# Kernel tuning notes

Measured on AMD Instinct MI355X. Metric: run time of the kernel, lower is better.

The kernel has to match this reference:

```python
import jax, jax.numpy as jnp
import numpy as np

BN_EPS = 1e-5


def setup_inputs() -> dict:
    key = jax.random.key(0)
    ks = jax.random.split(key, 6)
    n, c, h, w = 16, 256, 80, 80
    mip = max(8, c // 32)  # reduction=32 -> mip=8
    x = jax.random.normal(ks[0], (n, c, h, w), dtype=jnp.float32)
    # 1x1 conv weights (bias=False), stored as [out_ch, in_ch]
    w_fc = jax.random.normal(ks[1], (mip, c), dtype=jnp.float32) * (1.0 / np.sqrt(c))
    w_h = jax.random.normal(ks[2], (c, mip), dtype=jnp.float32) * (1.0 / np.sqrt(mip))
    w_w = jax.random.normal(ks[3], (c, mip), dtype=jnp.float32) * (1.0 / np.sqrt(mip))
    # BatchNorm2d(mip) inference params
    bn_gamma = jnp.ones((mip,), dtype=jnp.float32)
    bn_beta = jnp.zeros((mip,), dtype=jnp.float32)
    bn_mean = jax.random.normal(ks[4], (mip,), dtype=jnp.float32) * 0.1
    bn_var = jax.random.uniform(ks[5], (mip,), dtype=jnp.float32, minval=0.5, maxval=1.5)
    return {"x": x, "w_fc": w_fc, "bn_gamma": bn_gamma, "bn_beta": bn_beta,
            "bn_mean": bn_mean, "bn_var": bn_var, "w_h": w_h, "w_w": w_w}


def reference(x, w_fc, bn_gamma, bn_beta, bn_mean, bn_var, w_h, w_w):
    n, c, h, w = x.shape
    # Adaptive pools: pool_h -> mean over W (n,c,h); pool_w -> mean over H (n,c,w)
    x_h = jnp.mean(x, axis=3)  # (n, c, h)
    x_w = jnp.mean(x, axis=2)  # (n, c, w)
    # concat along the length axis (equiv. to torch cat on dim=2 after permute)
    y = jnp.concatenate([x_h, x_w], axis=2)  # (n, c, h+w)
    # fc: 1x1 conv c->mip + BN (inference) + SiLU
    y = jnp.einsum('mc,ncl->nml', w_fc, y)  # (n, mip, h+w)
    inv = bn_gamma / jnp.sqrt(bn_var + BN_EPS)
    y = y * inv[None, :, None] + (bn_beta - bn_mean * inv)[None, :, None]
    y = y * jax.nn.sigmoid(y)  # SiLU
    y_h, y_w = y[:, :, :h], y[:, :, h:]  # (n, mip, h), (n, mip, w)
    a_h = jax.nn.sigmoid(jnp.einsum('cm,nml->ncl', w_h, y_h))  # (n, c, h)
    a_w = jax.nn.sigmoid(jnp.einsum('cm,nml->ncl', w_w, y_w))  # (n, c, w)
    return x * a_h[:, :, :, None] * a_w[:, :, None, :]
```

## Files before the change

### kernel.cpp

```cpp
#include <hip/hip_runtime.h>

#define N_   16
#define C_   256
#define H_   80
#define W_   80
#define MIP_ 8
#define L_   160

__device__ __forceinline__ float bf2f(unsigned short b) {
    union { unsigned int u; float f; } v; v.u = ((unsigned int)b) << 16; return v.f;
}
__device__ __forceinline__ float gload(const void* p, int i, bool f32) {
    return f32 ? ((const float*)p)[i] : bf2f(((const unsigned short*)p)[i]);
}
__device__ __forceinline__ bool probe_f32(const void* g) {
    return *(const unsigned int*)g == 0x3F800000u;
}

__global__ __launch_bounds__(256) void pool_kernel(const void* __restrict__ x,
                                                   const void* __restrict__ g,
                                                   float* __restrict__ pooled) {
    __shared__ float lds[H_ * 81];
    const int b   = blockIdx.x;
    const int n   = b >> 8;
    const int cch = b & 255;
    const int t   = threadIdx.x;
    const bool f32 = probe_f32(g);

    if (f32) {
        const float4* pv = reinterpret_cast<const float4*>((const float*)x + (size_t)b * (H_ * W_));
        for (int v = t; v < 1600; v += 256) {
            float4 q = pv[v];
            int row  = v / 20;
            int col0 = (v - row * 20) * 4;
            float* dst = &lds[row * 81 + col0];
            dst[0] = q.x; dst[1] = q.y; dst[2] = q.z; dst[3] = q.w;
        }
    } else {
        const uint4* pv = reinterpret_cast<const uint4*>((const unsigned short*)x + (size_t)b * (H_ * W_));
        for (int v = t; v < 800; v += 256) {
            uint4 q = pv[v];
            int row  = v / 10;
            int col0 = (v - row * 10) * 8;
            float* dst = &lds[row * 81 + col0];
            unsigned int ws[4] = {q.x, q.y, q.z, q.w};
            #pragma unroll
            for (int i = 0; i < 4; ++i) {
                dst[2 * i]     = bf2f((unsigned short)(ws[i] & 0xffffu));
                dst[2 * i + 1] = bf2f((unsigned short)(ws[i] >> 16));
            }
        }
    }
    __syncthreads();

    if (t < H_) {
        float s0 = 0.f, s1 = 0.f, s2 = 0.f, s3 = 0.f;
        const float* r = &lds[t * 81];
        #pragma unroll
        for (int c4 = 0; c4 < W_; c4 += 4) {
            s0 += r[c4]; s1 += r[c4 + 1]; s2 += r[c4 + 2]; s3 += r[c4 + 3];
        }
        pooled[((size_t)n * L_ + t) * C_ + cch] = (s0 + s1 + s2 + s3) * (1.0f / (float)W_);
    } else if (t >= 128 && t < 128 + W_) {
        const int j = t - 128;
        float s0 = 0.f, s1 = 0.f, s2 = 0.f, s3 = 0.f;
        #pragma unroll
        for (int r4 = 0; r4 < H_; r4 += 4) {
            s0 += lds[(r4    ) * 81 + j];
            s1 += lds[(r4 + 1) * 81 + j];
            s2 += lds[(r4 + 2) * 81 + j];
            s3 += lds[(r4 + 3) * 81 + j];
        }
        pooled[((size_t)n * L_ + H_ + j) * C_ + cch] = (s0 + s1 + s2 + s3) * (1.0f / (float)H_);
    }
}

__global__ __launch_bounds__(256) void mid_kernel(const float* __restrict__ pooled,
                                                  const void* __restrict__ w_fc,
                                                  const void* __restrict__ g,
                                                  const void* __restrict__ be,
                                                  const void* __restrict__ mu,
                                                  const void* __restrict__ va,
                                                  const void* __restrict__ w_h,
                                                  const void* __restrict__ w_w,
                                                  float* __restrict__ a) {
    __shared__ float red[4 * MIP_];
    __shared__ float ysh[MIP_];
    const int b    = blockIdx.x;
    const int n    = b / L_;
    const int l    = b - n * L_;
    const int c    = threadIdx.x;
    const int lane = c & 63;
    const int wid  = c >> 6;
    const bool f32 = probe_f32(g);

    const float p = pooled[(size_t)b * C_ + c];

    #pragma unroll
    for (int m = 0; m < MIP_; ++m) {
        float v = gload(w_fc, m * C_ + c, f32) * p;
        #pragma unroll
        for (int off = 32; off > 0; off >>= 1) v += __shfl_down(v, off, 64);
        if (lane == 0) red[wid * MIP_ + m] = v;
    }
    __syncthreads();

    if (c < MIP_) {
        float y   = red[c] + red[MIP_ + c] + red[2 * MIP_ + c] + red[3 * MIP_ + c];
        float inv = gload(g, c, f32) * rsqrtf(gload(va, c, f32) + 1e-5f);
        y = y * inv + (gload(be, c, f32) - gload(mu, c, f32) * inv);
        ysh[c] = y / (1.0f + expf(-y));
    }
    __syncthreads();

    const void* wsel = (l < H_) ? w_h : w_w;
    float s = 0.f;
    #pragma unroll
    for (int m = 0; m < MIP_; ++m) s += gload(wsel, c * MIP_ + m, f32) * ysh[m];
    a[((size_t)n * C_ + c) * L_ + l] = 1.0f / (1.0f + expf(-s));
}

__global__ __launch_bounds__(256) void apply_kernel(const void* __restrict__ x,
                                                    const float* __restrict__ a,
                                                    const void* __restrict__ g,
                                                    float* __restrict__ out) {
    __shared__ float lah[H_];
    __shared__ float law[W_];
    const int b = blockIdx.x;
    const int t = threadIdx.x;
    if (t < L_) {
        float v = a[(size_t)b * L_ + t];
        if (t < H_) lah[t] = v; else law[t - H_] = v;
    }
    __syncthreads();
    const bool f32 = probe_f32(g);

    float4* ov = reinterpret_cast<float4*>(out + (size_t)b * (H_ * W_));
    if (f32) {
        const float4* xv = reinterpret_cast<const float4*>((const float*)x + (size_t)b * (H_ * W_));
        for (int v = t; v < 1600; v += 256) {
            float4 q = xv[v];
            int row  = v / 20;
            int col0 = (v - row * 20) * 4;
            const float ah = lah[row];
            float4 o;
            o.x = q.x * ah * law[col0    ];
            o.y = q.y * ah * law[col0 + 1];
            o.z = q.z * ah * law[col0 + 2];
            o.w = q.w * ah * law[col0 + 3];
            ov[v] = o;
        }
    } else {
        const uint4* xv = reinterpret_cast<const uint4*>((const unsigned short*)x + (size_t)b * (H_ * W_));
        for (int v = t; v < 800; v += 256) {
            uint4 q = xv[v];
            int row  = v / 10;
            int col0 = (v - row * 10) * 8;
            const float ah = lah[row];
            unsigned int ws[4] = {q.x, q.y, q.z, q.w};
            float4 o0, o1;
            o0.x = bf2f((unsigned short)(ws[0] & 0xffffu)) * ah * law[col0    ];
            o0.y = bf2f((unsigned short)(ws[0] >> 16))     * ah * law[col0 + 1];
            o0.z = bf2f((unsigned short)(ws[1] & 0xffffu)) * ah * law[col0 + 2];
            o0.w = bf2f((unsigned short)(ws[1] >> 16))     * ah * law[col0 + 3];
            o1.x = bf2f((unsigned short)(ws[2] & 0xffffu)) * ah * law[col0 + 4];
            o1.y = bf2f((unsigned short)(ws[2] >> 16))     * ah * law[col0 + 5];
            o1.z = bf2f((unsigned short)(ws[3] & 0xffffu)) * ah * law[col0 + 6];
            o1.w = bf2f((unsigned short)(ws[3] >> 16))     * ah * law[col0 + 7];
            ov[2 * v]     = o0;
            ov[2 * v + 1] = o1;
        }
    }
}

extern "C" void kernel_launch(void* const* d_in, const int* in_sizes, int n_in,
                              void* d_out, int out_size, void* d_ws, size_t ws_size,
                              hipStream_t stream) {
    const void* x    = d_in[0];
    const void* w_fc = d_in[1];
    const void* g    = d_in[2];
    const void* be   = d_in[3];
    const void* mu   = d_in[4];
    const void* va   = d_in[5];
    const void* w_h  = d_in[6];
    const void* w_w  = d_in[7];
    float* out = (float*)d_out;

    float* pooled = (float*)d_ws;
    float* a      = pooled + (size_t)N_ * L_ * C_;

    pool_kernel <<<N_ * C_, 256, 0, stream>>>(x, g, pooled);
    mid_kernel  <<<N_ * L_, 256, 0, stream>>>(pooled, w_fc, g, be, mu, va, w_h, w_w, a);
    apply_kernel<<<N_ * C_, 256, 0, stream>>>(x, a, g, out);
}
```

Before: 238.4 us.

## Move gate expansion into apply kernel and drop bf16 dtype-probe paths

Removes the runtime fp32/bf16 probe and the bf16 branches, so every kernel assumes fp32 inputs. The pooled layout changes so each pool block writes its 160 outputs contiguously instead of strided by C, and mid_kernel now reads with a stride. The second 1x1 conv and sigmoid move from mid_kernel into apply_kernel, which computes its 160 gates from the 8-wide y vectors. This removes the strided write of the full gate tensor and fixes the x-loading loops at 7 unrolled iterations. In exchange mid_kernel now does strided pooled reads, and apply_kernel repeats a little gate arithmetic per block.

Result: faster. 221.9 us (-6.9%).

```diff
diff --git a/kernel.cpp b/kernel.cpp
--- a/kernel.cpp
+++ b/kernel.cpp
@@ -7,52 +7,27 @@
 #define MIP_ 8
 #define L_   160
 
-__device__ __forceinline__ float bf2f(unsigned short b) {
-    union { unsigned int u; float f; } v; v.u = ((unsigned int)b) << 16; return v.f;
-}
-__device__ __forceinline__ float gload(const void* p, int i, bool f32) {
-    return f32 ? ((const float*)p)[i] : bf2f(((const unsigned short*)p)[i]);
-}
-__device__ __forceinline__ bool probe_f32(const void* g) {
-    return *(const unsigned int*)g == 0x3F800000u;
-}
-
-__global__ __launch_bounds__(256) void pool_kernel(const void* __restrict__ x,
-                                                   const void* __restrict__ g,
+__global__ __launch_bounds__(256) void pool_kernel(const float* __restrict__ x,
                                                    float* __restrict__ pooled) {
     __shared__ float lds[H_ * 81];
-    const int b   = blockIdx.x;
-    const int n   = b >> 8;
-    const int cch = b & 255;
-    const int t   = threadIdx.x;
-    const bool f32 = probe_f32(g);
+    const int b = blockIdx.x;
+    const int t = threadIdx.x;
 
-    if (f32) {
-        const float4* pv = reinterpret_cast<const float4*>((const float*)x + (size_t)b * (H_ * W_));
-        for (int v = t; v < 1600; v += 256) {
+    const float4* pv = reinterpret_cast<const float4*>(x + (size_t)b * (H_ * W_));
+    #pragma unroll
+    for (int it = 0; it < 7; ++it) {
+        int v = t + it * 256;
+        if (v < 1600) {
             float4 q = pv[v];
             int row  = v / 20;
             int col0 = (v - row * 20) * 4;
             float* dst = &lds[row * 81 + col0];
             dst[0] = q.x; dst[1] = q.y; dst[2] = q.z; dst[3] = q.w;
         }
-    } else {
-        const uint4* pv = reinterpret_cast<const uint4*>((const unsigned short*)x + (size_t)b * (H_ * W_));
-        for (int v = t; v < 800; v += 256) {
-            uint4 q = pv[v];
-            int row  = v / 10;
-            int col0 = (v - row * 10) * 8;
-            float* dst = &lds[row * 81 + col0];
-            unsigned int ws[4] = {q.x, q.y, q.z, q.w};
-            #pragma unroll
-            for (int i = 0; i < 4; ++i) {
-                dst[2 * i]     = bf2f((unsigned short)(ws[i] & 0xffffu));
-                dst[2 * i + 1] = bf2f((unsigned short)(ws[i] >> 16));
-            }
-        }
     }
     __syncthreads();
 
+    float* outp = pooled + (size_t)b * L_;
     if (t < H_) {
         float s0 = 0.f, s1 = 0.f, s2 = 0.f, s3 = 0.f;
         const float* r = &lds[t * 81];
@@ -60,7 +35,7 @@
         for (int c4 = 0; c4 < W_; c4 += 4) {
             s0 += r[c4]; s1 += r[c4 + 1]; s2 += r[c4 + 2]; s3 += r[c4 + 3];
         }
-        pooled[((size_t)n * L_ + t) * C_ + cch] = (s0 + s1 + s2 + s3) * (1.0f / (float)W_);
+        outp[t] = (s0 + s1 + s2 + s3) * (1.0f / (float)W_);
     } else if (t >= 128 && t < 128 + W_) {
         const int j = t - 128;
         float s0 = 0.f, s1 = 0.f, s2 = 0.f, s3 = 0.f;
@@ -71,34 +46,30 @@
             s2 += lds[(r4 + 2) * 81 + j];
             s3 += lds[(r4 + 3) * 81 + j];
         }
-        pooled[((size_t)n * L_ + H_ + j) * C_ + cch] = (s0 + s1 + s2 + s3) * (1.0f / (float)H_);
+        outp[H_ + j] = (s0 + s1 + s2 + s3) * (1.0f / (float)H_);
     }
 }
 
 __global__ __launch_bounds__(256) void mid_kernel(const float* __restrict__ pooled,
-                                                  const void* __restrict__ w_fc,
-                                                  const void* __restrict__ g,
-                                                  const void* __restrict__ be,
-                                                  const void* __restrict__ mu,
-                                                  const void* __restrict__ va,
-                                                  const void* __restrict__ w_h,
-                                                  const void* __restrict__ w_w,
-                                                  float* __restrict__ a) {
+                                                  const float* __restrict__ w_fc,
+                                                  const float* __restrict__ g,
+                                                  const float* __restrict__ be,
+                                                  const float* __restrict__ mu,
+                                                  const float* __restrict__ va,
+                                                  float* __restrict__ y_out) {
     __shared__ float red[4 * MIP_];
-    __shared__ float ysh[MIP_];
     const int b    = blockIdx.x;
     const int n    = b / L_;
     const int l    = b - n * L_;
     const int c    = threadIdx.x;
     const int lane = c & 63;
     const int wid  = c >> 6;
-    const bool f32 = probe_f32(g);
 
-    const float p = pooled[(size_t)b * C_ + c];
+    const float p = pooled[((size_t)n * C_ + c) * L_ + l];
 
     #pragma unroll
     for (int m = 0; m < MIP_; ++m) {
-        float v = gload(w_fc, m * C_ + c, f32) * p;
+        float v = w_fc[m * C_ + c] * p;
         #pragma unroll
         for (int off = 32; off > 0; off >>= 1) v += __shfl_down(v, off, 64);
         if (lane == 0) red[wid * MIP_ + m] = v;
@@ -107,38 +78,42 @@
 
     if (c < MIP_) {
         float y   = red[c] + red[MIP_ + c] + red[2 * MIP_ + c] + red[3 * MIP_ + c];
-        float inv = gload(g, c, f32) * rsqrtf(gload(va, c, f32) + 1e-5f);
-        y = y * inv + (gload(be, c, f32) - gload(mu, c, f32) * inv);
-        ysh[c] = y / (1.0f + expf(-y));
+        float inv = g[c] * rsqrtf(va[c] + 1e-5f);
+        y = y * inv + (be[c] - mu[c] * inv);
+        y_out[(size_t)b * MIP_ + c] = y / (1.0f + expf(-y));
     }
-    __syncthreads();
-
-    const void* wsel = (l < H_) ? w_h : w_w;
-    float s = 0.f;
-    #pragma unroll
-    for (int m = 0; m < MIP_; ++m) s += gload(wsel, c * MIP_ + m, f32) * ysh[m];
-    a[((size_t)n * C_ + c) * L_ + l] = 1.0f / (1.0f + expf(-s));
 }
 
-__global__ __launch_bounds__(256) void apply_kernel(const void* __restrict__ x,
-                                                    const float* __restrict__ a,
-                                                    const void* __restrict__ g,
+__global__ __launch_bounds__(256) void apply_kernel(const float* __restrict__ x,
+                                                    const float* __restrict__ y,
+                                                    const float* __restrict__ w_h,
+                                                    const float* __restrict__ w_w,
                                                     float* __restrict__ out) {
     __shared__ float lah[H_];
     __shared__ float law[W_];
     const int b = blockIdx.x;
+    const int n = b >> 8;
+    const int c = b & 255;
     const int t = threadIdx.x;
+
     if (t < L_) {
-        float v = a[(size_t)b * L_ + t];
-        if (t < H_) lah[t] = v; else law[t - H_] = v;
+        const float4* yp = reinterpret_cast<const float4*>(y + ((size_t)n * L_ + t) * MIP_);
+        const float4* wp = reinterpret_cast<const float4*>(((t < H_) ? w_h : w_w) + c * MIP_);
+        float4 y0 = yp[0], y1 = yp[1];
+        float4 w0 = wp[0], w1 = wp[1];
+        float s = y0.x * w0.x + y0.y * w0.y + y0.z * w0.z + y0.w * w0.w
+                + y1.x * w1.x + y1.y * w1.y + y1.z * w1.z + y1.w * w1.w;
+        float gate = 1.0f / (1.0f + expf(-s));
+        if (t < H_) lah[t] = gate; else law[t - H_] = gate;
     }
     __syncthreads();
-    const bool f32 = probe_f32(g);
 
-    float4* ov = reinterpret_cast<float4*>(out + (size_t)b * (H_ * W_));
-    if (f32) {
-        const float4* xv = reinterpret_cast<const float4*>((const float*)x + (size_t)b * (H_ * W_));
-        for (int v = t; v < 1600; v += 256) {
+    const float4* xv = reinterpret_cast<const float4*>(x + (size_t)b * (H_ * W_));
+    float4*       ov = reinterpret_cast<float4*>(out + (size_t)b * (H_ * W_));
+    #pragma unroll
+    for (int it = 0; it < 7; ++it) {
+        int v = t + it * 256;
+        if (v < 1600) {
             float4 q = xv[v];
             int row  = v / 20;
             int col0 = (v - row * 20) * 4;
@@ -150,46 +125,26 @@
             o.w = q.w * ah * law[col0 + 3];
             ov[v] = o;
         }
-    } else {
-        const uint4* xv = reinterpret_cast<const uint4*>((const unsigned short*)x + (size_t)b * (H_ * W_));
-        for (int v = t; v < 800; v += 256) {
-            uint4 q = xv[v];
-            int row  = v / 10;
-            int col0 = (v - row * 10) * 8;
-            const float ah = lah[row];
-            unsigned int ws[4] = {q.x, q.y, q.z, q.w};
-            float4 o0, o1;
-            o0.x = bf2f((unsigned short)(ws[0] & 0xffffu)) * ah * law[col0    ];
-            o0.y = bf2f((unsigned short)(ws[0] >> 16))     * ah * law[col0 + 1];
-            o0.z = bf2f((unsigned short)(ws[1] & 0xffffu)) * ah * law[col0 + 2];
-            o0.w = bf2f((unsigned short)(ws[1] >> 16))     * ah * law[col0 + 3];
-            o1.x = bf2f((unsigned short)(ws[2] & 0xffffu)) * ah * law[col0 + 4];
-            o1.y = bf2f((unsigned short)(ws[2] >> 16))     * ah * law[col0 + 5];
-            o1.z = bf2f((unsigned short)(ws[3] & 0xffffu)) * ah * law[col0 + 6];
-            o1.w = bf2f((unsigned short)(ws[3] >> 16))     * ah * law[col0 + 7];
-            ov[2 * v]     = o0;
-            ov[2 * v + 1] = o1;
-        }
     }
 }
 
 extern "C" void kernel_launch(void* const* d_in, const int* in_sizes, int n_in,
                               void* d_out, int out_size, void* d_ws, size_t ws_size,
                               hipStream_t stream) {
-    const void* x    = d_in[0];
-    const void* w_fc = d_in[1];
-    const void* g    = d_in[2];
-    const void* be   = d_in[3];
-    const void* mu   = d_in[4];
-    const void* va   = d_in[5];
-    const void* w_h  = d_in[6];
-    const void* w_w  = d_in[7];
+    const float* x    = (const float*)d_in[0];
+    const float* w_fc = (const float*)d_in[1];
+    const float* g    = (const float*)d_in[2];
+    const float* be   = (const float*)d_in[3];
+    const float* mu   = (const float*)d_in[4];
+    const float* va   = (const float*)d_in[5];
+    const float* w_h  = (const float*)d_in[6];
+    const float* w_w  = (const float*)d_in[7];
     float* out = (float*)d_out;
 
     float* pooled = (float*)d_ws;
-    float* a      = pooled + (size_t)N_ * L_ * C_;
+    float* y      = pooled + (size_t)N_ * C_ * L_;
 
-    pool_kernel <<<N_ * C_, 256, 0, stream>>>(x, g, pooled);
-    mid_kernel  <<<N_ * L_, 256, 0, stream>>>(pooled, w_fc, g, be, mu, va, w_h, w_w, a);
-    apply_kernel<<<N_ * C_, 256, 0, stream>>>(x, a, g, out);
+    pool_kernel <<<N_ * C_, 256, 0, stream>>>(x, pooled);
+    mid_kernel  <<<N_ * L_, 256, 0, stream>>>(pooled, w_fc, g, be, mu, va, y);
+    apply_kernel<<<N_ * C_, 256, 0, stream>>>(x, y, w_h, w_w, out);
 }
```
